# Performance work log

Measured on AMD Instinct MI355X. Metric: run time of the kernel, lower is better.

## Reference

```python
import jax, jax.numpy as jnp
import numpy as np

B, T, D = 4, 4096, 1024
LN_EPS = 1e-5

def _xavier(key, shape, gain=1.0):
    fan_in, fan_out = shape[1], shape[0]
    a = gain * np.sqrt(6.0 / (fan_in + fan_out))
    return jax.random.uniform(key, shape, jnp.float32, -a, a)

def setup_inputs() -> dict:
    key = jax.random.key(0)
    kx, kg, kv, ko = jax.random.split(key, 4)
    # log_decay param init so that softplus(log_decay) == decay_init (0.01)
    log_decay = jnp.asarray(np.log(np.expm1(0.01)), jnp.float32)
    return {
        "x": jax.random.normal(kx, (B, T, D), jnp.float32),
        "ln_w": jnp.ones((D,), jnp.float32),
        "ln_b": jnp.zeros((D,), jnp.float32),
        "gate_w": _xavier(kg, (D, D)),            # torch Linear weight [out, in]
        "gate_b": jnp.zeros((D,), jnp.float32),
        "value_w": _xavier(kv, (D, D), gain=0.01),
        "value_b": jnp.zeros((D,), jnp.float32),
        "out_w": _xavier(ko, (D, D), gain=0.01),
        "out_b": jnp.zeros((D,), jnp.float32),
        "log_decay": log_decay,
    }

def reference(x, ln_w, ln_b, gate_w, gate_b, value_w, value_b, out_w, out_b, log_decay):
    # LayerNorm over last dim
    mu = jnp.mean(x, axis=-1, keepdims=True)
    var = jnp.mean(jnp.square(x - mu), axis=-1, keepdims=True)
    normed = (x - mu) * jax.lax.rsqrt(var + LN_EPS) * ln_w + ln_b
    # gate / value projections (torch Linear: y = x @ W.T + b)
    g = jax.nn.sigmoid(normed @ gate_w.T + gate_b)
    v = normed @ value_w.T + value_b
    # push-pull: cumsum(g*v) - cumsum((1-g)*v) == cumsum((2g-1)*v)
    cumsum = jnp.cumsum((2.0 * g - 1.0) * v, axis=1)
    alpha = jax.nn.softplus(log_decay)
    positions = jnp.arange(T, dtype=jnp.float32)
    decay = jnp.exp(-alpha * positions)[None, :, None]  # [1, T, 1]
    output = cumsum * decay
    return x + (output @ out_w.T + out_b)
```

## Files before the change

### kernel.cpp

```cpp
#include <hip/hip_runtime.h>
#include <hip/hip_bf16.h>

#define BB 4
#define TT 4096
#define DD 1024
#define MM (BB * TT)
#define LN_EPS 1e-5f

#define NC 64
#define CL 64

typedef __attribute__((ext_vector_type(8))) short bf16x8;
typedef __attribute__((ext_vector_type(4))) float f32x4;

__device__ __forceinline__ float bfbits2f(unsigned short h) {
    return __uint_as_float(((unsigned int)h) << 16);
}
__device__ __forceinline__ unsigned short f2bfbits(float f) {
    __hip_bfloat16 h = __float2bfloat16(f);
    return *reinterpret_cast<unsigned short*>(&h);
}
__device__ __forceinline__ unsigned int pack2(float a, float b) {
    return (unsigned int)f2bfbits(a) | ((unsigned int)f2bfbits(b) << 16);
}

__device__ __forceinline__ void async_copy16(void* lds, const void* g) {
    __builtin_amdgcn_global_load_lds(
        (const __attribute__((address_space(1))) void*)g,
        (__attribute__((address_space(3))) void*)lds,
        16, 0, 0);
}

__global__ __launch_bounds__(256)
void convert_w3(const float* __restrict__ s0, const float* __restrict__ s1,
                const float* __restrict__ s2,
                __hip_bfloat16* __restrict__ d0, __hip_bfloat16* __restrict__ d1,
                __hip_bfloat16* __restrict__ d2)
{
    const int blk = blockIdx.x;
    const int w = blk >> 10;
    const float* src = (w == 0) ? s0 : (w == 1) ? s1 : s2;
    __hip_bfloat16* dst = (w == 0) ? d0 : (w == 1) ? d1 : d2;
    const size_t i = ((size_t)(blk & 1023) * 256 + threadIdx.x) * 4;
    float4 v = *(const float4*)(src + i);
    uint2 o;
    o.x = pack2(v.x, v.y);
    o.y = pack2(v.z, v.w);
    *(uint2*)((unsigned short*)dst + i) = o;
}

__global__ __launch_bounds__(256)
void ln_kernel(const float* __restrict__ x,
               const float* __restrict__ w,
               const float* __restrict__ b,
               __hip_bfloat16* __restrict__ out)
{
    const int wv   = threadIdx.x >> 6;
    const int lane = threadIdx.x & 63;
    const int row  = blockIdx.x * 4 + wv;

    const float* xr = x + (size_t)row * DD + lane * 16;
    float4 v[4];
    #pragma unroll
    for (int i = 0; i < 4; ++i) v[i] = *(const float4*)(xr + i * 4);

    float s = 0.0f, ss = 0.0f;
    #pragma unroll
    for (int i = 0; i < 4; ++i) {
        s  += (v[i].x + v[i].y) + (v[i].z + v[i].w);
        ss += fmaf(v[i].x, v[i].x, fmaf(v[i].y, v[i].y,
              fmaf(v[i].z, v[i].z, v[i].w * v[i].w)));
    }
    #pragma unroll
    for (int o = 32; o > 0; o >>= 1) {
        s  += __shfl_down(s, o);
        ss += __shfl_down(ss, o);
    }
    s  = __shfl(s, 0);
    ss = __shfl(ss, 0);

    const float mu   = s * (1.0f / DD);
    const float var  = ss * (1.0f / DD) - mu * mu;
    const float rstd = rsqrtf(var + LN_EPS);

    unsigned int res[8];
    #pragma unroll
    for (int i = 0; i < 4; ++i) {
        float4 wr = *(const float4*)(w + lane * 16 + i * 4);
        float4 br = *(const float4*)(b + lane * 16 + i * 4);
        float o0 = (v[i].x - mu) * rstd * wr.x + br.x;
        float o1 = (v[i].y - mu) * rstd * wr.y + br.y;
        float o2 = (v[i].z - mu) * rstd * wr.z + br.z;
        float o3 = (v[i].w - mu) * rstd * wr.w + br.w;
        res[i * 2]     = pack2(o0, o1);
        res[i * 2 + 1] = pack2(o2, o3);
    }
    unsigned short* op = (unsigned short*)out + (size_t)row * DD + lane * 16;
    *(uint4*)op       = make_uint4(res[0], res[1], res[2], res[3]);
    *(uint4*)(op + 8) = make_uint4(res[4], res[5], res[6], res[7]);
}

__global__ __launch_bounds__(512, 2)
void dual_gemm_gate(const __hip_bfloat16* __restrict__ A,
                    const __hip_bfloat16* __restrict__ Wg,
                    const __hip_bfloat16* __restrict__ Wv,
                    const float* __restrict__ gb,
                    const float* __restrict__ vb,
                    __hip_bfloat16* __restrict__ U,
                    float* __restrict__ Pk,
                    int M, int N, int K)
{
    constexpr int BK = 64;
    constexpr int NT = DD / BK;
    __shared__ short ring[3][3][128 * BK];

    const int tid  = threadIdx.x;
    const int m0   = blockIdx.x * 128;
    const int n0   = blockIdx.y * 128;
    const int wave = tid >> 6;
    const int lane = tid & 63;
    const int wm   = (wave & 1) * 64;
    const int wn   = (wave >> 1) * 32;
    const int lrow = lane & 15;
    const int kgrp = lane >> 4;
    const int swz  = lrow & 7;

    f32x4 accg[4][2] = {};
    f32x4 accv[4][2] = {};

    const __hip_bfloat16* gA[2];
    const __hip_bfloat16* gG[2];
    const __hip_bfloat16* gV[2];
    #pragma unroll
    for (int r = 0; r < 2; ++r) {
        const int slot = r * 512 + tid;
        const int srow = slot >> 3;
        const int gcc  = (slot & 7) ^ (srow & 7);
        gA[r] = A  + (size_t)(m0 + srow) * K + gcc * 8;
        gG[r] = Wg + (size_t)(n0 + srow) * K + gcc * 8;
        gV[r] = Wv + (size_t)(n0 + srow) * K + gcc * 8;
    }

    auto stage = [&](int sbuf, int kofs) {
        #pragma unroll
        for (int r = 0; r < 2; ++r) {
            const int so = (r * 512 + tid) * 8;
            async_copy16(&ring[sbuf][0][so], gA[r] + kofs);
            async_copy16(&ring[sbuf][1][so], gG[r] + kofs);
            async_copy16(&ring[sbuf][2][so], gV[r] + kofs);
        }
    };

    stage(0, 0);
    stage(1, BK);
    asm volatile("s_waitcnt vmcnt(6)\n\ts_barrier" ::: "memory");

    int rb = 0, sb = 2;
    for (int t = 0; t < NT; ++t) {
        if (t < NT - 2) stage(sb, (t + 2) * BK);

        const short* As = ring[rb][0];
        const short* Bg = ring[rb][1];
        const short* Bv = ring[rb][2];
        #pragma unroll
        for (int ks = 0; ks < 2; ++ks) {
            const int co = ((ks * 4 + kgrp) ^ swz) * 8;
            bf16x8 af[4], bgf[2], bvf[2];
            #pragma unroll
            for (int i = 0; i < 4; ++i)
                af[i] = *(const bf16x8*)&As[(wm + i * 16 + lrow) * BK + co];
            #pragma unroll
            for (int j = 0; j < 2; ++j) {
                bgf[j] = *(const bf16x8*)&Bg[(wn + j * 16 + lrow) * BK + co];
                bvf[j] = *(const bf16x8*)&Bv[(wn + j * 16 + lrow) * BK + co];
            }
            __builtin_amdgcn_s_setprio(1);
            #pragma unroll
            for (int i = 0; i < 4; ++i)
                #pragma unroll
                for (int j = 0; j < 2; ++j) {
                    accg[i][j] = __builtin_amdgcn_mfma_f32_16x16x32_bf16(
                        bgf[j], af[i], accg[i][j], 0, 0, 0);
                    accv[i][j] = __builtin_amdgcn_mfma_f32_16x16x32_bf16(
                        bvf[j], af[i], accv[i][j], 0, 0, 0);
                }
            __builtin_amdgcn_s_setprio(0);
        }

        if (t < NT - 2)
            asm volatile("s_waitcnt vmcnt(6)\n\ts_barrier" ::: "memory");
        else if (t == NT - 2)
            asm volatile("s_waitcnt vmcnt(0)\n\ts_barrier" ::: "memory");
        rb = (rb == 2) ? 0 : rb + 1;
        sb = (sb == 2) ? 0 : sb + 1;
    }

    const int chrow = m0 + wm;
    const int cb    = chrow >> 12;
    const int cc    = (chrow & (TT - 1)) >> 6;

    #pragma unroll
    for (int j = 0; j < 2; ++j) {
        const int nb = n0 + wn + j * 16 + kgrp * 4;
        const float4 gb4 = *(const float4*)(gb + nb);
        const float4 vb4 = *(const float4*)(vb + nb);
        float4 ps = make_float4(0.f, 0.f, 0.f, 0.f);
        #pragma unroll
        for (int i = 0; i < 4; ++i) {
            const int m = m0 + wm + i * 16 + lrow;
            const float g0 = accg[i][j][0] + gb4.x, v0 = accv[i][j][0] + vb4.x;
            const float g1 = accg[i][j][1] + gb4.y, v1 = accv[i][j][1] + vb4.y;
            const float g2 = accg[i][j][2] + gb4.z, v2 = accv[i][j][2] + vb4.z;
            const float g3 = accg[i][j][3] + gb4.w, v3 = accv[i][j][3] + vb4.w;
            const float u0 = (2.0f / (1.0f + __expf(-g0)) - 1.0f) * v0;
            const float u1 = (2.0f / (1.0f + __expf(-g1)) - 1.0f) * v1;
            const float u2 = (2.0f / (1.0f + __expf(-g2)) - 1.0f) * v2;
            const float u3 = (2.0f / (1.0f + __expf(-g3)) - 1.0f) * v3;
            ps.x += u0; ps.y += u1; ps.z += u2; ps.w += u3;
            uint2 o;
            o.x = pack2(u0, u1);
            o.y = pack2(u2, u3);
            *(uint2*)((unsigned short*)U + (size_t)m * N + nb) = o;
        }
        #pragma unroll
        for (int mk = 1; mk <= 8; mk <<= 1) {
            ps.x += __shfl_xor(ps.x, mk);
            ps.y += __shfl_xor(ps.y, mk);
            ps.z += __shfl_xor(ps.z, mk);
            ps.w += __shfl_xor(ps.w, mk);
        }
        if (lrow == 0)
            *(float4*)&Pk[((size_t)cb * NC + cc) * DD + nb] = ps;
    }
}

__global__ __launch_bounds__(512, 2)
void gemm_out(const __hip_bfloat16* __restrict__ A,
              const __hip_bfloat16* __restrict__ W,
              const float* __restrict__ bias,
              const float* __restrict__ X,
              float* __restrict__ C,
              int M, int N, int K)
{
    constexpr int BK = 64;
    constexpr int NT = DD / BK;
    __shared__ short As_[3][256 * BK];
    __shared__ short Bs_[3][128 * BK];

    const int tid  = threadIdx.x;
    const int m0   = blockIdx.x * 256;
    const int n0   = blockIdx.y * 128;
    const int wave = tid >> 6;
    const int lane = tid & 63;
    const int wm   = (wave & 3) * 64;
    const int wn   = (wave >> 2) * 64;
    const int lrow = lane & 15;
    const int kgrp = lane >> 4;
    const int swz  = lrow & 7;

    f32x4 acc[4][4] = {};

    const __hip_bfloat16* gA[4];
    const __hip_bfloat16* gB[2];
    #pragma unroll
    for (int r = 0; r < 4; ++r) {
        const int slot = r * 512 + tid;
        const int srow = slot >> 3;
        const int gcc  = (slot & 7) ^ (srow & 7);
        gA[r] = A + (size_t)(m0 + srow) * K + gcc * 8;
    }
    #pragma unroll
    for (int r = 0; r < 2; ++r) {
        const int slot = r * 512 + tid;
        const int srow = slot >> 3;
        const int gcc  = (slot & 7) ^ (srow & 7);
        gB[r] = W + (size_t)(n0 + srow) * K + gcc * 8;
    }

    auto stage = [&](int sbuf, int kofs) {
        #pragma unroll
        for (int r = 0; r < 4; ++r)
            async_copy16(&As_[sbuf][(r * 512 + tid) * 8], gA[r] + kofs);
        #pragma unroll
        for (int r = 0; r < 2; ++r)
            async_copy16(&Bs_[sbuf][(r * 512 + tid) * 8], gB[r] + kofs);
    };

    stage(0, 0);
    stage(1, BK);
    asm volatile("s_waitcnt vmcnt(6)\n\ts_barrier" ::: "memory");

    int rb = 0, sb = 2;
    for (int t = 0; t < NT; ++t) {
        if (t < NT - 2) stage(sb, (t + 2) * BK);

        const short* As = As_[rb];
        const short* Bs = Bs_[rb];
        #pragma unroll
        for (int ks = 0; ks < 2; ++ks) {
            const int co = ((ks * 4 + kgrp) ^ swz) * 8;
            bf16x8 af[4], bfr[4];
            #pragma unroll
            for (int i = 0; i < 4; ++i)
                af[i] = *(const bf16x8*)&As[(wm + i * 16 + lrow) * BK + co];
            #pragma unroll
            for (int j = 0; j < 4; ++j)
                bfr[j] = *(const bf16x8*)&Bs[(wn + j * 16 + lrow) * BK + co];
            __builtin_amdgcn_s_setprio(1);
            #pragma unroll
            for (int i = 0; i < 4; ++i)
                #pragma unroll
                for (int j = 0; j < 4; ++j)
                    acc[i][j] = __builtin_amdgcn_mfma_f32_16x16x32_bf16(
                        bfr[j], af[i], acc[i][j], 0, 0, 0);
            __builtin_amdgcn_s_setprio(0);
        }

        if (t < NT - 2)
            asm volatile("s_waitcnt vmcnt(6)\n\ts_barrier" ::: "memory");
        else if (t == NT - 2)
            asm volatile("s_waitcnt vmcnt(0)\n\ts_barrier" ::: "memory");
        rb = (rb == 2) ? 0 : rb + 1;
        sb = (sb == 2) ? 0 : sb + 1;
    }

    #pragma unroll
    for (int j = 0; j < 4; ++j) {
        const int nb = n0 + wn + j * 16 + kgrp * 4;
        const float4 bv = *(const float4*)(bias + nb);
        #pragma unroll
        for (int i = 0; i < 4; ++i) {
            const int m = m0 + wm + i * 16 + lrow;
            const size_t idx = (size_t)m * N + nb;
            const float4 xv = *(const float4*)(X + idx);
            float4 o;
            o.x = acc[i][j][0] + bv.x + xv.x;
            o.y = acc[i][j][1] + bv.y + xv.y;
            o.z = acc[i][j][2] + bv.z + xv.z;
            o.w = acc[i][j][3] + bv.w + xv.w;
            *(float4*)(C + idx) = o;
        }
    }
}

__global__ __launch_bounds__(256)
void scan_offsets(float* __restrict__ Pk)
{
    __shared__ float Tl[64][68];
    __shared__ float Seg[4][64];

    const int tid  = threadIdx.x;
    const int col0 = blockIdx.x * 64;
    const int b    = col0 >> 10;
    const int d0   = col0 & 1023;

    #pragma unroll
    for (int r = 0; r < 4; ++r) {
        const int idx = r * 256 + tid;
        const int c = idx >> 4, q = idx & 15;
        float4 v = *(const float4*)&Pk[((size_t)b * NC + c) * DD + d0 + q * 4];
        *(float4*)&Tl[c][q * 4] = v;
    }
    __syncthreads();

    const int j = tid & 63, seg = tid >> 6;
    float ssum = 0.0f;
    #pragma unroll
    for (int k = 0; k < 16; ++k) ssum += Tl[seg * 16 + k][j];
    Seg[seg][j] = ssum;
    __syncthreads();

    float run = 0.0f;
    for (int s = 0; s < seg; ++s) run += Seg[s][j];
    #pragma unroll
    for (int k = 0; k < 16; ++k) {
        const int c = seg * 16 + k;
        const float v = Tl[c][j];
        Tl[c][j] = run;
        run += v;
    }
    __syncthreads();

    #pragma unroll
    for (int r = 0; r < 4; ++r) {
        const int idx = r * 256 + tid;
        const int c = idx >> 4, q = idx & 15;
        *(float4*)&Pk[((size_t)b * NC + c) * DD + d0 + q * 4] =
            *(const float4*)&Tl[c][q * 4];
    }
}

__global__ __launch_bounds__(128)
void scan_final(const __hip_bfloat16* __restrict__ U,
                const float* __restrict__ Pk,
                const float* __restrict__ log_decay,
                __hip_bfloat16* __restrict__ S)
{
    const int c = blockIdx.x, b = blockIdx.y;
    const int d8 = threadIdx.x * 8;

    const float ld = log_decay[0];
    const float alpha = log1pf(__expf(ld));
    const float ratio = __expf(-alpha);
    float dec = __expf(-alpha * (float)(c * CL));

    const float* pk = &Pk[((size_t)b * NC + c) * DD + d8];
    float run[8];
    float4 r0 = *(const float4*)pk;
    float4 r1 = *(const float4*)(pk + 4);
    run[0] = r0.x; run[1] = r0.y; run[2] = r0.z; run[3] = r0.w;
    run[4] = r1.x; run[5] = r1.y; run[6] = r1.z; run[7] = r1.w;

    const size_t base = ((size_t)b * TT + (size_t)c * CL) * DD + d8;
    const unsigned short* up = (const unsigned short*)U + base;
    unsigned short* sp = (unsigned short*)S + base;

    #pragma unroll 8
    for (int t = 0; t < CL; ++t) {
        uint4 raw = *(const uint4*)(up + (size_t)t * DD);
        unsigned int wds[4] = {raw.x, raw.y, raw.z, raw.w};
        uint4 o;
        unsigned int* ow = (unsigned int*)&o;
        #pragma unroll
        for (int k = 0; k < 4; ++k) {
            run[2 * k]     += bfbits2f((unsigned short)(wds[k] & 0xFFFF));
            run[2 * k + 1] += bfbits2f((unsigned short)(wds[k] >> 16));
            ow[k] = pack2(run[2 * k] * dec, run[2 * k + 1] * dec);
        }
        *(uint4*)(sp + (size_t)t * DD) = o;
        dec *= ratio;
    }
}

extern "C" void kernel_launch(void* const* d_in, const int* in_sizes, int n_in,
                              void* d_out, int out_size, void* d_ws, size_t ws_size,
                              hipStream_t stream)
{
    const float* x        = (const float*)d_in[0];
    const float* ln_w     = (const float*)d_in[1];
    const float* ln_b     = (const float*)d_in[2];
    const float* gate_w   = (const float*)d_in[3];
    const float* gate_b   = (const float*)d_in[4];
    const float* value_w  = (const float*)d_in[5];
    const float* value_b  = (const float*)d_in[6];
    const float* out_w    = (const float*)d_in[7];
    const float* out_b    = (const float*)d_in[8];
    const float* log_dec  = (const float*)d_in[9];
    float* out = (float*)d_out;

    char* ws = (char*)d_ws;
    const size_t MB = 1024 * 1024;
    __hip_bfloat16* normed = (__hip_bfloat16*)(ws);
    __hip_bfloat16* S      = (__hip_bfloat16*)(ws);
    float*          Pk     = (float*)(ws + 32 * MB);
    __hip_bfloat16* Wg16   = (__hip_bfloat16*)(ws + 33 * MB);
    __hip_bfloat16* Wv16   = (__hip_bfloat16*)(ws + 35 * MB);
    __hip_bfloat16* Wo16   = (__hip_bfloat16*)(ws + 37 * MB);
    __hip_bfloat16* U      = (__hip_bfloat16*)d_out;

    convert_w3<<<dim3(3072), dim3(256), 0, stream>>>(
        gate_w, value_w, out_w, Wg16, Wv16, Wo16);

    ln_kernel<<<dim3(MM / 4), dim3(256), 0, stream>>>(x, ln_w, ln_b, normed);

    dual_gemm_gate<<<dim3(MM / 128, DD / 128), dim3(512), 0, stream>>>(
        normed, Wg16, Wv16, gate_b, value_b, U, Pk, MM, DD, DD);

    scan_offsets<<<dim3(NC), dim3(256), 0, stream>>>(Pk);
    scan_final<<<dim3(NC, BB), dim3(128), 0, stream>>>(U, Pk, log_dec, S);

    gemm_out<<<dim3(MM / 256, DD / 128), dim3(512), 0, stream>>>(
        S, Wo16, out_b, x, out, MM, DD, DD);
}
```

Before: 302.2 us.

## Interleave half-tile async prefetch with MFMA sub-steps in both GEMM kernels

```diff
diff --git a/kernel.cpp b/kernel.cpp
--- a/kernel.cpp
+++ b/kernel.cpp
@@ -141,27 +141,24 @@
         gV[r] = Wv + (size_t)(n0 + srow) * K + gcc * 8;
     }
 
-    auto stage = [&](int sbuf, int kofs) {
-        #pragma unroll
-        for (int r = 0; r < 2; ++r) {
-            const int so = (r * 512 + tid) * 8;
-            async_copy16(&ring[sbuf][0][so], gA[r] + kofs);
-            async_copy16(&ring[sbuf][1][so], gG[r] + kofs);
-            async_copy16(&ring[sbuf][2][so], gV[r] + kofs);
-        }
+    auto stage_half = [&](int sbuf, int kofs, int h) {
+        const int so = (h * 512 + tid) * 8;
+        async_copy16(&ring[sbuf][0][so], gA[h] + kofs);
+        async_copy16(&ring[sbuf][1][so], gG[h] + kofs);
+        async_copy16(&ring[sbuf][2][so], gV[h] + kofs);
     };
 
-    stage(0, 0);
-    stage(1, BK);
+    stage_half(0, 0, 0);  stage_half(0, 0, 1);
+    stage_half(1, BK, 0); stage_half(1, BK, 1);
     asm volatile("s_waitcnt vmcnt(6)\n\ts_barrier" ::: "memory");
 
     int rb = 0, sb = 2;
     for (int t = 0; t < NT; ++t) {
-        if (t < NT - 2) stage(sb, (t + 2) * BK);
-
         const short* As = ring[rb][0];
         const short* Bg = ring[rb][1];
         const short* Bv = ring[rb][2];
+        const int kof2 = (t + 2) * BK;
+
         #pragma unroll
         for (int ks = 0; ks < 2; ++ks) {
             const int co = ((ks * 4 + kgrp) ^ swz) * 8;
@@ -174,6 +171,14 @@
                 bgf[j] = *(const bf16x8*)&Bg[(wn + j * 16 + lrow) * BK + co];
                 bvf[j] = *(const bf16x8*)&Bv[(wn + j * 16 + lrow) * BK + co];
             }
+            if (t < NT - 2) stage_half(sb, kof2, ks);
+            if (ks == 1) {
+                if (t < NT - 2)
+                    asm volatile("s_waitcnt vmcnt(6)" ::: "memory");
+                else if (t == NT - 2)
+                    asm volatile("s_waitcnt vmcnt(0)" ::: "memory");
+            }
+            asm volatile("s_barrier" ::: "memory");
             __builtin_amdgcn_s_setprio(1);
             #pragma unroll
             for (int i = 0; i < 4; ++i)
@@ -185,12 +190,8 @@
                         bvf[j], af[i], accv[i][j], 0, 0, 0);
                 }
             __builtin_amdgcn_s_setprio(0);
-        }
-
-        if (t < NT - 2)
-            asm volatile("s_waitcnt vmcnt(6)\n\ts_barrier" ::: "memory");
-        else if (t == NT - 2)
-            asm volatile("s_waitcnt vmcnt(0)\n\ts_barrier" ::: "memory");
+            asm volatile("s_barrier" ::: "memory");
+        }
         rb = (rb == 2) ? 0 : rb + 1;
         sb = (sb == 2) ? 0 : sb + 1;
     }
@@ -244,8 +245,8 @@
 {
     constexpr int BK = 64;
     constexpr int NT = DD / BK;
-    __shared__ short As_[3][256 * BK];
-    __shared__ short Bs_[3][128 * BK];
+    __shared__ short Aring[3][256 * BK];
+    __shared__ short Bring[3][128 * BK];
 
     const int tid  = threadIdx.x;
     const int m0   = blockIdx.x * 256;
@@ -277,25 +278,22 @@
         gB[r] = W + (size_t)(n0 + srow) * K + gcc * 8;
     }
 
-    auto stage = [&](int sbuf, int kofs) {
-        #pragma unroll
-        for (int r = 0; r < 4; ++r)
-            async_copy16(&As_[sbuf][(r * 512 + tid) * 8], gA[r] + kofs);
-        #pragma unroll
-        for (int r = 0; r < 2; ++r)
-            async_copy16(&Bs_[sbuf][(r * 512 + tid) * 8], gB[r] + kofs);
+    auto stage_half = [&](int sbuf, int kofs, int h) {
+        async_copy16(&Aring[sbuf][((h * 2) * 512 + tid) * 8],     gA[h * 2] + kofs);
+        async_copy16(&Aring[sbuf][((h * 2 + 1) * 512 + tid) * 8], gA[h * 2 + 1] + kofs);
+        async_copy16(&Bring[sbuf][(h * 512 + tid) * 8],           gB[h] + kofs);
     };
 
-    stage(0, 0);
-    stage(1, BK);
+    stage_half(0, 0, 0);  stage_half(0, 0, 1);
+    stage_half(1, BK, 0); stage_half(1, BK, 1);
     asm volatile("s_waitcnt vmcnt(6)\n\ts_barrier" ::: "memory");
 
     int rb = 0, sb = 2;
     for (int t = 0; t < NT; ++t) {
-        if (t < NT - 2) stage(sb, (t + 2) * BK);
-
-        const short* As = As_[rb];
-        const short* Bs = Bs_[rb];
+        const short* As = Aring[rb];
+        const short* Bs = Bring[rb];
+        const int kof2 = (t + 2) * BK;
+
         #pragma unroll
         for (int ks = 0; ks < 2; ++ks) {
             const int co = ((ks * 4 + kgrp) ^ swz) * 8;
@@ -306,6 +304,14 @@
             #pragma unroll
             for (int j = 0; j < 4; ++j)
                 bfr[j] = *(const bf16x8*)&Bs[(wn + j * 16 + lrow) * BK + co];
+            if (t < NT - 2) stage_half(sb, kof2, ks);
+            if (ks == 1) {
+                if (t < NT - 2)
+                    asm volatile("s_waitcnt vmcnt(6)" ::: "memory");
+                else if (t == NT - 2)
+                    asm volatile("s_waitcnt vmcnt(0)" ::: "memory");
+            }
+            asm volatile("s_barrier" ::: "memory");
             __builtin_amdgcn_s_setprio(1);
             #pragma unroll
             for (int i = 0; i < 4; ++i)
@@ -314,12 +320,8 @@
                     acc[i][j] = __builtin_amdgcn_mfma_f32_16x16x32_bf16(
                         bfr[j], af[i], acc[i][j], 0, 0, 0);
             __builtin_amdgcn_s_setprio(0);
-        }
-
-        if (t < NT - 2)
-            asm volatile("s_waitcnt vmcnt(6)\n\ts_barrier" ::: "memory");
-        else if (t == NT - 2)
-            asm volatile("s_waitcnt vmcnt(0)\n\ts_barrier" ::: "memory");
+            asm volatile("s_barrier" ::: "memory");
+        }
         rb = (rb == 2) ? 0 : rb + 1;
         sb = (sb == 2) ? 0 : sb + 1;
     }
```

New measurement: 294.6 us. 2.5% less time.
